# Performance work log

Measured on AMD Instinct MI355X. Metric: run time of the kernel, lower is better.

The kernel has to match this reference:

```python
import jax, jax.numpy as jnp
import numpy as np

# ---- config (mirrors cfg / init kwargs) ----
FEAT_STRIDE = 16
IM_DIMS = (1024, 1024)          # (height, width)
ANCHOR_SCALES = (8, 16, 32)
ANCHOR_RATIOS = (0.5, 1.0, 2.0)
PRE_NMS_TOPN = 6000             # eval mode (cfg_key=1)
POST_NMS_TOPN = 300
NMS_THRESH = 0.7
MIN_SIZE = 16


def _generate_base_anchors(base_size=16, ratios=ANCHOR_RATIOS, scales=ANCHOR_SCALES):
    """py-faster-rcnn generate_anchors, in numpy (static)."""
    def mk(ws, hs, xc, yc):
        return np.stack([xc - 0.5 * (ws - 1), yc - 0.5 * (hs - 1),
                         xc + 0.5 * (ws - 1), yc + 0.5 * (hs - 1)], axis=1)
    base = np.array([0, 0, base_size - 1, base_size - 1], dtype=np.float64)
    w = base[2] - base[0] + 1; h = base[3] - base[1] + 1
    xc = base[0] + 0.5 * (w - 1); yc = base[1] + 0.5 * (h - 1)
    # ratio enum
    size = w * h
    ws = np.round(np.sqrt(size / np.array(ratios)))
    hs = np.round(ws * np.array(ratios))
    ratio_anchors = mk(ws, hs, xc, yc)
    # scale enum
    out = []
    for a in ratio_anchors:
        aw = a[2] - a[0] + 1; ah = a[3] - a[1] + 1
        axc = a[0] + 0.5 * (aw - 1); ayc = a[1] + 0.5 * (ah - 1)
        out.append(mk(aw * np.array(scales), ah * np.array(scales), axc, ayc))
    return np.concatenate(out, axis=0).astype(np.float32)  # [A,4]


def _all_anchors(H, W):
    base = _generate_base_anchors()                       # [A,4]
    sx = np.arange(W) * FEAT_STRIDE
    sy = np.arange(H) * FEAT_STRIDE
    sx, sy = np.meshgrid(sx, sy)
    shifts = np.stack([sx.ravel(), sy.ravel(), sx.ravel(), sy.ravel()], axis=1)  # [H*W,4]
    anchors = shifts[:, None, :].astype(np.float32) + base[None, :, :]
    return anchors.reshape(-1, 4)                         # [H*W*A, 4]


def setup_inputs() -> dict:
    key = jax.random.key(0)
    k1, k2 = jax.random.split(key)
    H, W, A = 64, 64, 9
    rpn_cls_score = jax.random.normal(k1, (1, H, W, 2 * A), dtype=jnp.float32)
    rpn_bbox_pred = jax.random.normal(k2, (1, H, W, 4 * A), dtype=jnp.float32)
    return {"rpn_cls_score": rpn_cls_score, "rpn_bbox_pred": rpn_bbox_pred}


def _proposals(rpn_cls_score, rpn_bbox_pred):
    _, H, W, C2 = rpn_cls_score.shape
    A = C2 // 2
    # rpn_softmax: per-anchor 2-way softmax, foreground prob
    scores = jax.nn.softmax(rpn_cls_score.reshape(H, W, A, 2), axis=-1)[..., 1].reshape(-1)  # [N]
    deltas = rpn_bbox_pred.reshape(-1, 4)                  # [N,4]
    anchors = jnp.asarray(_all_anchors(H, W))              # [N,4]
    # bbox_transform_inv
    aw = anchors[:, 2] - anchors[:, 0] + 1.0
    ah = anchors[:, 3] - anchors[:, 1] + 1.0
    axc = anchors[:, 0] + 0.5 * aw
    ayc = anchors[:, 1] + 0.5 * ah
    dx, dy, dw, dh = deltas[:, 0], deltas[:, 1], deltas[:, 2], deltas[:, 3]
    pxc = dx * aw + axc; pyc = dy * ah + ayc
    pw = jnp.exp(dw) * aw; ph = jnp.exp(dh) * ah
    x1 = pxc - 0.5 * pw; y1 = pyc - 0.5 * ph
    x2 = pxc + 0.5 * pw; y2 = pyc + 0.5 * ph
    # clip to image
    im_h, im_w = IM_DIMS
    x1 = jnp.clip(x1, 0.0, im_w - 1.0); x2 = jnp.clip(x2, 0.0, im_w - 1.0)
    y1 = jnp.clip(y1, 0.0, im_h - 1.0); y2 = jnp.clip(y2, 0.0, im_h - 1.0)
    boxes = jnp.stack([x1, y1, x2, y2], axis=1)            # [N,4]
    # filter too-small boxes by masking their score
    valid = ((x2 - x1 + 1.0) >= MIN_SIZE) & ((y2 - y1 + 1.0) >= MIN_SIZE)
    scores = jnp.where(valid, scores, -jnp.inf)
    return boxes, scores


def _nms_keep(boxes, K):
    """Greedy NMS keep-mask over score-descending boxes [K,4]."""
    x1, y1, x2, y2 = boxes[:, 0], boxes[:, 1], boxes[:, 2], boxes[:, 3]
    areas = (x2 - x1 + 1.0) * (y2 - y1 + 1.0)
    ix1 = jnp.maximum(x1[:, None], x1[None, :])
    iy1 = jnp.maximum(y1[:, None], y1[None, :])
    ix2 = jnp.minimum(x2[:, None], x2[None, :])
    iy2 = jnp.minimum(y2[:, None], y2[None, :])
    iw = jnp.maximum(ix2 - ix1 + 1.0, 0.0)
    ih = jnp.maximum(iy2 - iy1 + 1.0, 0.0)
    inter = iw * ih
    iou = inter / (areas[:, None] + areas[None, :] - inter)  # [K,K]
    idxs = jnp.arange(K)
    def body(i, keep):
        sup = keep[i] & (iou[i] > NMS_THRESH) & (idxs > i)
        return keep & ~sup
    return jax.lax.fori_loop(0, K, body, jnp.ones((K,), bool))


def reference(rpn_cls_score, rpn_bbox_pred):
    boxes, scores = _proposals(rpn_cls_score, rpn_bbox_pred)
    K = min(PRE_NMS_TOPN, scores.shape[0])
    top_scores, order = jax.lax.top_k(scores, K)           # score-descending
    top_boxes = boxes[order]                               # [K,4]
    keep = _nms_keep(top_boxes, K)
    sel_scores = jnp.where(keep, top_scores, -jnp.inf)
    _, idx = jax.lax.top_k(sel_scores, POST_NMS_TOPN)      # kept, in score order
    out_boxes = top_boxes[idx]                             # [post,4]
    blob = jnp.concatenate([jnp.zeros((POST_NMS_TOPN, 1), out_boxes.dtype), out_boxes], axis=1)
    return blob                                            # [post,5] (batch_idx, x1,y1,x2,y2)
```

## Files before the change

### kernel.cpp

```cpp
#include <hip/hip_runtime.h>
#include <stdint.h>

typedef unsigned long long u64;
typedef unsigned int u32;

#define N_ANCH 36864
#define WGRID 64
#define A_PER 9
#define KTOP 6000
#define NOUT 300
#define NBIN 5120
#define NCHK 94
#define NCH2 47
#define NJ   6016
#define INF_BIN 0
#define NMSW 4
#define SLOTS 10
#define SPILLCAP 64

#define BARRIER_LDS() do {                                   \
    asm volatile("s_waitcnt lgkmcnt(0)" ::: "memory");       \
    __builtin_amdgcn_s_barrier();                            \
    asm volatile("" ::: "memory");                           \
} while (0)

__constant__ float c_ax1[9] = {-84.f,-176.f,-360.f,-56.f,-120.f,-248.f,-36.f,-80.f,-168.f};
__constant__ float c_ay1[9] = {-40.f,-88.f,-184.f,-56.f,-120.f,-248.f,-80.f,-168.f,-344.f};
__constant__ float c_aw[9]  = {184.f,368.f,736.f,128.f,256.f,512.f,88.f,176.f,352.f};
__constant__ float c_ah[9]  = {96.f,192.f,384.f,128.f,256.f,512.f,176.f,352.f,704.f};

__device__ __forceinline__ u32 binof(u32 u) {
    if (u < 0x80000000u) return 0u;
    if (u < 0xBF000000u) return 1u + ((u - 0x80000000u) >> 22);
    return 256u + ((u - 0xBF000000u) >> 11);
}

__global__ __launch_bounds__(256) void proposal_kernel(const float* __restrict__ cls,
                                                       const float* __restrict__ dlt,
                                                       u64* __restrict__ keys,
                                                       float4* __restrict__ boxes,
                                                       u32* __restrict__ hist) {
    __shared__ u32 lh[NBIN];
    const int t = threadIdx.x;
    for (int b = t; b < NBIN; b += 256) lh[b] = 0;
    __syncthreads();

    int i = blockIdx.x * 256 + t;
    int a  = i % A_PER;
    int hw = i / A_PER;
    int wx = hw % WGRID;
    int hy = hw / WGRID;

    float2 lp = *(const float2*)(cls + hw * 18 + 2 * a);
    float l0 = lp.x, l1 = lp.y;
    float m  = fmaxf(l0, l1);
    float e0 = expf(l0 - m), e1 = expf(l1 - m);
    float s  = e1 / (e0 + e1);

    float4 dd = *(const float4*)(dlt + hw * 36 + 4 * a);
    float dx = dd.x, dy = dd.y, dw = dd.z, dh = dd.w;
    float aw = c_aw[a], ah = c_ah[a];
    float axc = (c_ax1[a] + 16.f * (float)wx) + 0.5f * aw;
    float ayc = (c_ay1[a] + 16.f * (float)hy) + 0.5f * ah;

    float pxc = dx * aw + axc;
    float pyc = dy * ah + ayc;
    float pw  = expf(dw) * aw;
    float ph  = expf(dh) * ah;
    float x1 = pxc - 0.5f * pw, y1 = pyc - 0.5f * ph;
    float x2 = pxc + 0.5f * pw, y2 = pyc + 0.5f * ph;
    x1 = fminf(fmaxf(x1, 0.f), 1023.f);
    x2 = fminf(fmaxf(x2, 0.f), 1023.f);
    y1 = fminf(fmaxf(y1, 0.f), 1023.f);
    y2 = fminf(fmaxf(y2, 0.f), 1023.f);
    bool valid = ((x2 - x1 + 1.f) >= 16.f) && ((y2 - y1 + 1.f) >= 16.f);
    float sc = valid ? s : -__builtin_huge_valf();

    u32 sb  = __float_as_uint(sc);
    u32 ord = (sb & 0x80000000u) ? ~sb : (sb | 0x80000000u);
    u64 key = ((u64)ord << 32) | (u32)(~(u32)i);
    keys[i]  = key;
    boxes[i] = make_float4(x1, y1, x2, y2);

    u64 infb = __ballot(!valid);
    if (valid) {
        atomicAdd(&lh[binof(ord)], 1u);
    } else {
        int lane = t & 63;
        if (lane == __builtin_ctzll(infb))
            atomicAdd(&lh[INF_BIN], (u32)__popcll(infb));
    }
    __syncthreads();
    for (int b = t; b < NBIN; b += 256) {
        u32 v = lh[b];
        if (v) atomicAdd(&hist[b], v);
    }
}

__global__ __launch_bounds__(1024) void scan_kernel(const u32* __restrict__ hist,
                                                    u32* __restrict__ binStart,
                                                    u32* __restrict__ gEV) {
    __shared__ u32 wsum[16];
    const int t = threadIdx.x;
    const int lane = t & 63;
    const int v = t >> 6;
    if (t == 0) gEV[1] = KTOP;
    int hi = NBIN - 1 - 5 * t;
    u32 cnt[5];
    u32 sum = 0;
#pragma unroll
    for (int k = 0; k < 5; ++k) { cnt[k] = hist[hi - k]; sum += cnt[k]; }
    u32 s = sum;
#pragma unroll
    for (int d = 1; d < 64; d <<= 1) {
        u32 x = __shfl_up(s, d, 64);
        if (lane >= d) s += x;
    }
    if (lane == 63) wsum[v] = s;
    __syncthreads();
    u32 base = 0;
#pragma unroll
    for (int q = 0; q < 16; ++q) {
        u32 x = wsum[q];
        if (q < v) base += x;
    }
    u32 run = base + s - sum;
#pragma unroll
    for (int k = 0; k < 5; ++k) {
        int b = hi - k;
        binStart[b] = run;
        u32 end = run + cnt[k];
        if (run < KTOP && end >= KTOP) gEV[0] = end;
        run = end;
    }
}

__global__ void scatter_kernel(const u64* __restrict__ keys,
                               const u32* __restrict__ binStart,
                               u32* __restrict__ cursor,
                               u64* __restrict__ scat) {
    int i = blockIdx.x * blockDim.x + threadIdx.x;
    if (i >= N_ANCH) return;
    u64 k = keys[i];
    u32 b = binof((u32)(k >> 32));
    u32 s = binStart[b];
    if (s < KTOP) {
        u32 p = s + atomicAdd(&cursor[b], 1u);
        scat[p] = k;
    }
}

__global__ void rank_kernel(const u64* __restrict__ scat,
                            const u32* __restrict__ binStart,
                            const u32* __restrict__ hist,
                            const float4* __restrict__ boxes,
                            const u32* __restrict__ gEV,
                            float4* __restrict__ topBoxes,
                            int* __restrict__ gV) {
    int i = blockIdx.x * blockDim.x + threadIdx.x;
    u32 E = gEV[0];
    if (i >= (int)E) return;
    u64 k = scat[i];
    u32 b = binof((u32)(k >> 32));
    u32 s = binStart[b], c = hist[b];
    u32 r = s;
    for (u32 j = s; j < s + c; ++j) r += (scat[j] > k) ? 1u : 0u;
    if (r < KTOP) {
        int idx = (int)(~(u32)k);
        topBoxes[r] = boxes[idx];
        if (!(k >> 63)) atomicMin(gV, (int)r);
    }
}

__device__ __forceinline__ bool iou_gt(float4 a, float areaA, float4 b, float areaB) {
    float ix1 = fmaxf(a.x, b.x), iy1 = fmaxf(a.y, b.y);
    float ix2 = fminf(a.z, b.z), iy2 = fminf(a.w, b.w);
    float iw = fmaxf(ix2 - ix1 + 1.0f, 0.0f);
    float ih = fmaxf(iy2 - iy1 + 1.0f, 0.0f);
    float inter = iw * ih;
    float iou = inter / (areaA + areaB - inter);
    return iou > 0.7f;
}

__global__ __launch_bounds__(256) void maskT_kernel(const float4* __restrict__ topBoxes,
                                                    const u32* __restrict__ gEV,
                                                    u64* __restrict__ S) {
    const int V = (int)gEV[1];
    const int nch = (V + 63) >> 6;
    const int jc = blockIdx.x;
    const int w0 = blockIdx.y * 4;
    if (jc >= nch || w0 > jc) return;
    __shared__ float4 cb[256];
    __shared__ float  ca[256];
    const int t = threadIdx.x;
    const int lane = t & 63;
    {
        int ci = w0 * 64 + t;
        float4 b = (ci < V) ? topBoxes[ci] : make_float4(0.f, 0.f, -8.f, -8.f);
        cb[t] = b;
        ca[t] = (b.z - b.x + 1.f) * (b.w - b.y + 1.f);
    }
    __syncthreads();
    const int w = w0 + (t >> 6);
    if (w > jc || w >= nch) return;
    const int j = jc * 64 + lane;
    float4 bj = (j < V) ? topBoxes[j] : make_float4(0.f, 0.f, -8.f, -8.f);
    float aj = (bj.z - bj.x + 1.f) * (bj.w - bj.y + 1.f);
    const int s0 = (t >> 6) * 64;
    u64 m = 0;
#pragma unroll 4
    for (int b = 0; b < 64; ++b)
        if (iou_gt(bj, aj, cb[s0 + b], ca[s0 + b])) m |= (1ull << b);
    if (w == jc) m &= ((1ull << lane) - 1ull);
    S[(u64)w * NJ + j] = m;
}

__global__ __launch_bounds__(256) void nms_out_kernel(const float4* __restrict__ topBoxes,
                                                      const u32* __restrict__ gEV,
                                                      const u64* __restrict__ S,
                                                      float* __restrict__ out) {
    __shared__ u64 dA[NCH2][64];
    __shared__ u64 dAB[NCH2][64];
    __shared__ u64 dB[NCH2][64];
    __shared__ u64 keepw[NCHK];
    __shared__ u64 supw[2][2 * NMSW];
    __shared__ u64 spillK[SPILLCAP];
    __shared__ u32 spillW[SPILLCAP];
    __shared__ u32 wsum[NMSW];
    const int t = threadIdx.x;
    const int lane = t & 63;
    const int v = t >> 6;
    const int V = (int)gEV[1];
    const int nch = (V + 63) >> 6;
    const int nr  = (nch + 1) >> 1;
    if (t < NCHK) keepw[t] = 0;
    for (int idx = t; idx < nr * 64; idx += 256) {
        int r = idx >> 6, l = idx & 63;
        dA[r][l]  = S[(u64)(2 * r) * NJ + 128 * r + l];
        dAB[r][l] = S[(u64)(2 * r) * NJ + 128 * r + 64 + l];
        dB[r][l]  = S[(u64)(2 * r + 1) * NJ + 128 * r + 64 + l];
    }
    __syncthreads();

    u64 kwS[SLOTS], pA[SLOTS], pB[SLOTS], aofs[SLOTS];
#pragma unroll
    for (int k = 0; k < SLOTS; ++k) { kwS[k] = 0; pA[k] = 0; pB[k] = 0; aofs[k] = 0; }
    int nslot = 0, nspill = 0, nkept = 0;

    for (int r = 0; r < nr; ++r) {
        const int par = r & 1;
        u64 accA = 0, accB = 0;
#pragma unroll
        for (int k = 0; k < SLOTS; ++k) {
            if (nslot > NMSW * k + v) { accA |= pA[k] & kwS[k]; accB |= pB[k] & kwS[k]; }
        }
        for (int s = v; s < nspill; s += NMSW) {
            u64 kk = spillK[s];
            const u64* row = S + (u64)spillW[s] * NJ + 128 * r + lane;
            accA |= row[0] & kk; accB |= row[64] & kk;
        }
        u64 bA = __ballot(accA != 0ull), bB = __ballot(accB != 0ull);
        if (lane == 0) { supw[par][v] = bA; supw[par][NMSW + v] = bB; }
        if (r + 1 < nr) {
            u64 ofsn = (u64)(128 * (r + 1)) + lane;
#pragma unroll
            for (int k = 0; k < SLOTS; ++k)
                if (nslot > NMSW * k + v) { pA[k] = S[aofs[k] + ofsn]; pB[k] = S[aofs[k] + ofsn + 64]; }
        }
        BARRIER_LDS();
        u64 rwA = supw[par][0] | supw[par][1] | supw[par][2] | supw[par][3];
        u64 rwB = supw[par][4] | supw[par][5] | supw[par][6] | supw[par][7];
        int remA = V - 128 * r;
        int remB = remA - 64;
        u64 aliveA = (remA >= 64) ? ~0ull : ((remA <= 0) ? 0ull : ((1ull << remA) - 1ull));
        u64 aliveB = (remB >= 64) ? ~0ull : ((remB <= 0) ? 0ull : ((1ull << remB) - 1ull));
        u64 dAl = dA[r][lane], dABl = dAB[r][lane], dBl = dB[r][lane];
        u64 candA = ~rwA & aliveA, kbA = 0;
        while (candA) {
            int b = __builtin_ctzll(candA);
            kbA |= (1ull << b);
            candA &= ~(1ull << b);
            candA &= ~__ballot(((dAl >> b) & 1ull) != 0ull);
        }
        u64 supAB = __ballot((dABl & kbA) != 0ull);
        u64 candB = ~(rwB | supAB) & aliveB, kbB = 0;
        while (candB) {
            int b = __builtin_ctzll(candB);
            kbB |= (1ull << b);
            candB &= ~(1ull << b);
            candB &= ~__ballot(((dBl >> b) & 1ull) != 0ull);
        }
        if (t == 0) { keepw[2 * r] = kbA; if (2 * r + 1 < nch) keepw[2 * r + 1] = kbB; }
        bool sadd = false;
        if (kbA) {
            int so = nslot & (NMSW - 1), si = nslot >> 2;
            if (si < SLOTS) {
                if (v == so) {
#pragma unroll
                    for (int k = 0; k < SLOTS; ++k) if (k == si) {
                        kwS[k] = kbA; aofs[k] = (u64)(2 * r) * NJ;
                        if (r + 1 < nr) {
                            u64 o = (u64)(128 * (r + 1)) + lane;
                            pA[k] = S[aofs[k] + o]; pB[k] = S[aofs[k] + o + 64];
                        }
                    }
                }
                ++nslot;
            } else if (nspill < SPILLCAP) {
                if (v == NMSW - 1 && lane == 0) { spillW[nspill] = 2 * r; spillK[nspill] = kbA; }
                ++nspill; sadd = true;
            }
        }
        if (kbB) {
            int so = nslot & (NMSW - 1), si = nslot >> 2;
            if (si < SLOTS) {
                if (v == so) {
#pragma unroll
                    for (int k = 0; k < SLOTS; ++k) if (k == si) {
                        kwS[k] = kbB; aofs[k] = (u64)(2 * r + 1) * NJ;
                        if (r + 1 < nr) {
                            u64 o = (u64)(128 * (r + 1)) + lane;
                            pA[k] = S[aofs[k] + o]; pB[k] = S[aofs[k] + o + 64];
                        }
                    }
                }
                ++nslot;
            } else if (nspill < SPILLCAP) {
                if (v == NMSW - 1 && lane == 0) { spillW[nspill] = 2 * r + 1; spillK[nspill] = kbB; }
                ++nspill; sadd = true;
            }
        }
        if (sadd) BARRIER_LDS();
        nkept += __popcll(kbA) + __popcll(kbB);
        if (nkept >= NOUT) break;
    }
    __syncthreads();

    const int per = 24;
    int r0 = t * per;
    int r1 = min(r0 + per, KTOP);
    u32 cnt = 0;
    for (int r = r0; r < r1; ++r)
        cnt += (u32)((keepw[r >> 6] >> (r & 63)) & 1ull);
    u32 s = cnt;
#pragma unroll
    for (int d = 1; d < 64; d <<= 1) {
        u32 x = __shfl_up(s, d, 64);
        if (lane >= d) s += x;
    }
    if (lane == 63) wsum[v] = s;
    __syncthreads();
    u32 base = 0;
    u32 total = 0;
#pragma unroll
    for (int q = 0; q < NMSW; ++q) {
        u32 x = wsum[q];
        if (q < v) base += x;
        total += x;
    }
    const int n1 = min((int)total, NOUT);
    int kp = (int)(base + s - cnt);
    for (int r = r0; r < r1; ++r) {
        int kept = (int)((keepw[r >> 6] >> (r & 63)) & 1ull);
        int pos = kept ? kp : (n1 + r - kp);
        if (pos < NOUT) {
            float4 b = topBoxes[r];
            out[pos * 5 + 0] = 0.f;
            out[pos * 5 + 1] = b.x;
            out[pos * 5 + 2] = b.y;
            out[pos * 5 + 3] = b.z;
            out[pos * 5 + 4] = b.w;
        }
        kp += kept;
    }
}

extern "C" void kernel_launch(void* const* d_in, const int* in_sizes, int n_in,
                              void* d_out, int out_size, void* d_ws, size_t ws_size,
                              hipStream_t stream) {
    const float* cls = (const float*)d_in[0];
    const float* dlt = (const float*)d_in[1];
    float* out = (float*)d_out;
    char* ws = (char*)d_ws;
    u64*    keys     = (u64*)   (ws);
    u64*    scat     = (u64*)   (ws + 294912);
    float4* boxes    = (float4*)(ws + 589824);
    float4* topBoxes = (float4*)(ws + 1179648);
    u32*    hist     = (u32*)   (ws + 1275648);
    u32*    cursor   = (u32*)   (ws + 1296128);
    u32*    binStart = (u32*)   (ws + 1316608);
    u32*    gEV      = (u32*)   (ws + 1337088);
    u64*    S        = (u64*)   (ws + 1337344);

    hipMemsetAsync(hist, 0, 2 * NBIN * sizeof(u32), stream);
    proposal_kernel<<<144, 256, 0, stream>>>(cls, dlt, keys, boxes, hist);
    scan_kernel<<<1, 1024, 0, stream>>>(hist, binStart, gEV);
    scatter_kernel<<<(N_ANCH + 255) / 256, 256, 0, stream>>>(keys, binStart, cursor, scat);
    rank_kernel<<<(N_ANCH + 255) / 256, 256, 0, stream>>>(scat, binStart, hist, boxes, gEV,
                                                          topBoxes, (int*)&gEV[1]);
    maskT_kernel<<<dim3(NCHK, (NCHK + 3) / 4), 256, 0, stream>>>(topBoxes, gEV, S);
    nms_out_kernel<<<1, 256, 0, stream>>>(topBoxes, gEV, S, out);
}
```

Measured before the change: 120.7 us.

## Fuse all proposal/NMS stages into one cooperative kernel with grid syncs

Replaces the memset plus six separate kernel launches with a single cooperative kernel of 144 blocks that runs every stage (proposal, histogram scan, scatter, rank, mask build, NMS/output) separated by grid-wide syncs. The goal is to remove per-launch overhead and inter-kernel gaps, which dominate such a small, latency-bound pipeline. The mask stage now uses a triangular task list with wave shuffles instead of LDS staging. The NMS loop holds slots in named registers and prefetches the diagonal blocks instead of preloading them into LDS. If the cooperative launch fails, it falls back to per-phase launches. Grid syncs have their own cost, and fewer blocks are now used for the mask stage.

```diff
diff --git a/kernel.cpp b/kernel.cpp
--- a/kernel.cpp
+++ b/kernel.cpp
@@ -1,5 +1,8 @@
 #include <hip/hip_runtime.h>
+#include <hip/hip_cooperative_groups.h>
 #include <stdint.h>
+
+namespace cg = cooperative_groups;
 
 typedef unsigned long long u64;
 typedef unsigned int u32;
@@ -11,11 +14,9 @@
 #define NOUT 300
 #define NBIN 5120
 #define NCHK 94
-#define NCH2 47
 #define NJ   6016
-#define INF_BIN 0
-#define NMSW 4
-#define SLOTS 10
+#define GRIDB 144
+#define NSLOT 12
 #define SPILLCAP 64
 
 #define BARRIER_LDS() do {                                   \
@@ -33,143 +34,6 @@
     if (u < 0x80000000u) return 0u;
     if (u < 0xBF000000u) return 1u + ((u - 0x80000000u) >> 22);
     return 256u + ((u - 0xBF000000u) >> 11);
-}
-
-__global__ __launch_bounds__(256) void proposal_kernel(const float* __restrict__ cls,
-                                                       const float* __restrict__ dlt,
-                                                       u64* __restrict__ keys,
-                                                       float4* __restrict__ boxes,
-                                                       u32* __restrict__ hist) {
-    __shared__ u32 lh[NBIN];
-    const int t = threadIdx.x;
-    for (int b = t; b < NBIN; b += 256) lh[b] = 0;
-    __syncthreads();
-
-    int i = blockIdx.x * 256 + t;
-    int a  = i % A_PER;
-    int hw = i / A_PER;
-    int wx = hw % WGRID;
-    int hy = hw / WGRID;
-
-    float2 lp = *(const float2*)(cls + hw * 18 + 2 * a);
-    float l0 = lp.x, l1 = lp.y;
-    float m  = fmaxf(l0, l1);
-    float e0 = expf(l0 - m), e1 = expf(l1 - m);
-    float s  = e1 / (e0 + e1);
-
-    float4 dd = *(const float4*)(dlt + hw * 36 + 4 * a);
-    float dx = dd.x, dy = dd.y, dw = dd.z, dh = dd.w;
-    float aw = c_aw[a], ah = c_ah[a];
-    float axc = (c_ax1[a] + 16.f * (float)wx) + 0.5f * aw;
-    float ayc = (c_ay1[a] + 16.f * (float)hy) + 0.5f * ah;
-
-    float pxc = dx * aw + axc;
-    float pyc = dy * ah + ayc;
-    float pw  = expf(dw) * aw;
-    float ph  = expf(dh) * ah;
-    float x1 = pxc - 0.5f * pw, y1 = pyc - 0.5f * ph;
-    float x2 = pxc + 0.5f * pw, y2 = pyc + 0.5f * ph;
-    x1 = fminf(fmaxf(x1, 0.f), 1023.f);
-    x2 = fminf(fmaxf(x2, 0.f), 1023.f);
-    y1 = fminf(fmaxf(y1, 0.f), 1023.f);
-    y2 = fminf(fmaxf(y2, 0.f), 1023.f);
-    bool valid = ((x2 - x1 + 1.f) >= 16.f) && ((y2 - y1 + 1.f) >= 16.f);
-    float sc = valid ? s : -__builtin_huge_valf();
-
-    u32 sb  = __float_as_uint(sc);
-    u32 ord = (sb & 0x80000000u) ? ~sb : (sb | 0x80000000u);
-    u64 key = ((u64)ord << 32) | (u32)(~(u32)i);
-    keys[i]  = key;
-    boxes[i] = make_float4(x1, y1, x2, y2);
-
-    u64 infb = __ballot(!valid);
-    if (valid) {
-        atomicAdd(&lh[binof(ord)], 1u);
-    } else {
-        int lane = t & 63;
-        if (lane == __builtin_ctzll(infb))
-            atomicAdd(&lh[INF_BIN], (u32)__popcll(infb));
-    }
-    __syncthreads();
-    for (int b = t; b < NBIN; b += 256) {
-        u32 v = lh[b];
-        if (v) atomicAdd(&hist[b], v);
-    }
-}
-
-__global__ __launch_bounds__(1024) void scan_kernel(const u32* __restrict__ hist,
-                                                    u32* __restrict__ binStart,
-                                                    u32* __restrict__ gEV) {
-    __shared__ u32 wsum[16];
-    const int t = threadIdx.x;
-    const int lane = t & 63;
-    const int v = t >> 6;
-    if (t == 0) gEV[1] = KTOP;
-    int hi = NBIN - 1 - 5 * t;
-    u32 cnt[5];
-    u32 sum = 0;
-#pragma unroll
-    for (int k = 0; k < 5; ++k) { cnt[k] = hist[hi - k]; sum += cnt[k]; }
-    u32 s = sum;
-#pragma unroll
-    for (int d = 1; d < 64; d <<= 1) {
-        u32 x = __shfl_up(s, d, 64);
-        if (lane >= d) s += x;
-    }
-    if (lane == 63) wsum[v] = s;
-    __syncthreads();
-    u32 base = 0;
-#pragma unroll
-    for (int q = 0; q < 16; ++q) {
-        u32 x = wsum[q];
-        if (q < v) base += x;
-    }
-    u32 run = base + s - sum;
-#pragma unroll
-    for (int k = 0; k < 5; ++k) {
-        int b = hi - k;
-        binStart[b] = run;
-        u32 end = run + cnt[k];
-        if (run < KTOP && end >= KTOP) gEV[0] = end;
-        run = end;
-    }
-}
-
-__global__ void scatter_kernel(const u64* __restrict__ keys,
-                               const u32* __restrict__ binStart,
-                               u32* __restrict__ cursor,
-                               u64* __restrict__ scat) {
-    int i = blockIdx.x * blockDim.x + threadIdx.x;
-    if (i >= N_ANCH) return;
-    u64 k = keys[i];
-    u32 b = binof((u32)(k >> 32));
-    u32 s = binStart[b];
-    if (s < KTOP) {
-        u32 p = s + atomicAdd(&cursor[b], 1u);
-        scat[p] = k;
-    }
-}
-
-__global__ void rank_kernel(const u64* __restrict__ scat,
-                            const u32* __restrict__ binStart,
-                            const u32* __restrict__ hist,
-                            const float4* __restrict__ boxes,
-                            const u32* __restrict__ gEV,
-                            float4* __restrict__ topBoxes,
-                            int* __restrict__ gV) {
-    int i = blockIdx.x * blockDim.x + threadIdx.x;
-    u32 E = gEV[0];
-    if (i >= (int)E) return;
-    u64 k = scat[i];
-    u32 b = binof((u32)(k >> 32));
-    u32 s = binStart[b], c = hist[b];
-    u32 r = s;
-    for (u32 j = s; j < s + c; ++j) r += (scat[j] > k) ? 1u : 0u;
-    if (r < KTOP) {
-        int idx = (int)(~(u32)k);
-        topBoxes[r] = boxes[idx];
-        if (!(k >> 63)) atomicMin(gV, (int)r);
-    }
 }
 
 __device__ __forceinline__ bool iou_gt(float4 a, float areaA, float4 b, float areaB) {
@@ -182,206 +46,36 @@
     return iou > 0.7f;
 }
 
-__global__ __launch_bounds__(256) void maskT_kernel(const float4* __restrict__ topBoxes,
-                                                    const u32* __restrict__ gEV,
-                                                    u64* __restrict__ S) {
-    const int V = (int)gEV[1];
-    const int nch = (V + 63) >> 6;
-    const int jc = blockIdx.x;
-    const int w0 = blockIdx.y * 4;
-    if (jc >= nch || w0 > jc) return;
-    __shared__ float4 cb[256];
-    __shared__ float  ca[256];
-    const int t = threadIdx.x;
-    const int lane = t & 63;
-    {
-        int ci = w0 * 64 + t;
-        float4 b = (ci < V) ? topBoxes[ci] : make_float4(0.f, 0.f, -8.f, -8.f);
-        cb[t] = b;
-        ca[t] = (b.z - b.x + 1.f) * (b.w - b.y + 1.f);
-    }
-    __syncthreads();
-    const int w = w0 + (t >> 6);
-    if (w > jc || w >= nch) return;
-    const int j = jc * 64 + lane;
-    float4 bj = (j < V) ? topBoxes[j] : make_float4(0.f, 0.f, -8.f, -8.f);
-    float aj = (bj.z - bj.x + 1.f) * (bj.w - bj.y + 1.f);
-    const int s0 = (t >> 6) * 64;
-    u64 m = 0;
-#pragma unroll 4
-    for (int b = 0; b < 64; ++b)
-        if (iou_gt(bj, aj, cb[s0 + b], ca[s0 + b])) m |= (1ull << b);
-    if (w == jc) m &= ((1ull << lane) - 1ull);
-    S[(u64)w * NJ + j] = m;
-}
-
-__global__ __launch_bounds__(256) void nms_out_kernel(const float4* __restrict__ topBoxes,
-                                                      const u32* __restrict__ gEV,
-                                                      const u64* __restrict__ S,
-                                                      float* __restrict__ out) {
-    __shared__ u64 dA[NCH2][64];
-    __shared__ u64 dAB[NCH2][64];
-    __shared__ u64 dB[NCH2][64];
-    __shared__ u64 keepw[NCHK];
-    __shared__ u64 supw[2][2 * NMSW];
-    __shared__ u64 spillK[SPILLCAP];
-    __shared__ u32 spillW[SPILLCAP];
-    __shared__ u32 wsum[NMSW];
-    const int t = threadIdx.x;
-    const int lane = t & 63;
-    const int v = t >> 6;
-    const int V = (int)gEV[1];
-    const int nch = (V + 63) >> 6;
-    const int nr  = (nch + 1) >> 1;
-    if (t < NCHK) keepw[t] = 0;
-    for (int idx = t; idx < nr * 64; idx += 256) {
-        int r = idx >> 6, l = idx & 63;
-        dA[r][l]  = S[(u64)(2 * r) * NJ + 128 * r + l];
-        dAB[r][l] = S[(u64)(2 * r) * NJ + 128 * r + 64 + l];
-        dB[r][l]  = S[(u64)(2 * r + 1) * NJ + 128 * r + 64 + l];
-    }
-    __syncthreads();
-
-    u64 kwS[SLOTS], pA[SLOTS], pB[SLOTS], aofs[SLOTS];
-#pragma unroll
-    for (int k = 0; k < SLOTS; ++k) { kwS[k] = 0; pA[k] = 0; pB[k] = 0; aofs[k] = 0; }
-    int nslot = 0, nspill = 0, nkept = 0;
-
-    for (int r = 0; r < nr; ++r) {
-        const int par = r & 1;
-        u64 accA = 0, accB = 0;
-#pragma unroll
-        for (int k = 0; k < SLOTS; ++k) {
-            if (nslot > NMSW * k + v) { accA |= pA[k] & kwS[k]; accB |= pB[k] & kwS[k]; }
-        }
-        for (int s = v; s < nspill; s += NMSW) {
-            u64 kk = spillK[s];
-            const u64* row = S + (u64)spillW[s] * NJ + 128 * r + lane;
-            accA |= row[0] & kk; accB |= row[64] & kk;
-        }
-        u64 bA = __ballot(accA != 0ull), bB = __ballot(accB != 0ull);
-        if (lane == 0) { supw[par][v] = bA; supw[par][NMSW + v] = bB; }
-        if (r + 1 < nr) {
-            u64 ofsn = (u64)(128 * (r + 1)) + lane;
-#pragma unroll
-            for (int k = 0; k < SLOTS; ++k)
-                if (nslot > NMSW * k + v) { pA[k] = S[aofs[k] + ofsn]; pB[k] = S[aofs[k] + ofsn + 64]; }
-        }
-        BARRIER_LDS();
-        u64 rwA = supw[par][0] | supw[par][1] | supw[par][2] | supw[par][3];
-        u64 rwB = supw[par][4] | supw[par][5] | supw[par][6] | supw[par][7];
-        int remA = V - 128 * r;
-        int remB = remA - 64;
-        u64 aliveA = (remA >= 64) ? ~0ull : ((remA <= 0) ? 0ull : ((1ull << remA) - 1ull));
-        u64 aliveB = (remB >= 64) ? ~0ull : ((remB <= 0) ? 0ull : ((1ull << remB) - 1ull));
-        u64 dAl = dA[r][lane], dABl = dAB[r][lane], dBl = dB[r][lane];
-        u64 candA = ~rwA & aliveA, kbA = 0;
-        while (candA) {
-            int b = __builtin_ctzll(candA);
-            kbA |= (1ull << b);
-            candA &= ~(1ull << b);
-            candA &= ~__ballot(((dAl >> b) & 1ull) != 0ull);
-        }
-        u64 supAB = __ballot((dABl & kbA) != 0ull);
-        u64 candB = ~(rwB | supAB) & aliveB, kbB = 0;
-        while (candB) {
-            int b = __builtin_ctzll(candB);
-            kbB |= (1ull << b);
-            candB &= ~(1ull << b);
-            candB &= ~__ballot(((dBl >> b) & 1ull) != 0ull);
-        }
-        if (t == 0) { keepw[2 * r] = kbA; if (2 * r + 1 < nch) keepw[2 * r + 1] = kbB; }
-        bool sadd = false;
-        if (kbA) {
-            int so = nslot & (NMSW - 1), si = nslot >> 2;
-            if (si < SLOTS) {
-                if (v == so) {
-#pragma unroll
-                    for (int k = 0; k < SLOTS; ++k) if (k == si) {
-                        kwS[k] = kbA; aofs[k] = (u64)(2 * r) * NJ;
-                        if (r + 1 < nr) {
-                            u64 o = (u64)(128 * (r + 1)) + lane;
-                            pA[k] = S[aofs[k] + o]; pB[k] = S[aofs[k] + o + 64];
-                        }
-                    }
-                }
-                ++nslot;
-            } else if (nspill < SPILLCAP) {
-                if (v == NMSW - 1 && lane == 0) { spillW[nspill] = 2 * r; spillK[nspill] = kbA; }
-                ++nspill; sadd = true;
-            }
-        }
-        if (kbB) {
-            int so = nslot & (NMSW - 1), si = nslot >> 2;
-            if (si < SLOTS) {
-                if (v == so) {
-#pragma unroll
-                    for (int k = 0; k < SLOTS; ++k) if (k == si) {
-                        kwS[k] = kbB; aofs[k] = (u64)(2 * r + 1) * NJ;
-                        if (r + 1 < nr) {
-                            u64 o = (u64)(128 * (r + 1)) + lane;
-                            pA[k] = S[aofs[k] + o]; pB[k] = S[aofs[k] + o + 64];
-                        }
-                    }
-                }
-                ++nslot;
-            } else if (nspill < SPILLCAP) {
-                if (v == NMSW - 1 && lane == 0) { spillW[nspill] = 2 * r + 1; spillK[nspill] = kbB; }
-                ++nspill; sadd = true;
-            }
-        }
-        if (sadd) BARRIER_LDS();
-        nkept += __popcll(kbA) + __popcll(kbB);
-        if (nkept >= NOUT) break;
-    }
-    __syncthreads();
-
-    const int per = 24;
-    int r0 = t * per;
-    int r1 = min(r0 + per, KTOP);
-    u32 cnt = 0;
-    for (int r = r0; r < r1; ++r)
-        cnt += (u32)((keepw[r >> 6] >> (r & 63)) & 1ull);
-    u32 s = cnt;
-#pragma unroll
-    for (int d = 1; d < 64; d <<= 1) {
-        u32 x = __shfl_up(s, d, 64);
-        if (lane >= d) s += x;
-    }
-    if (lane == 63) wsum[v] = s;
-    __syncthreads();
-    u32 base = 0;
-    u32 total = 0;
-#pragma unroll
-    for (int q = 0; q < NMSW; ++q) {
-        u32 x = wsum[q];
-        if (q < v) base += x;
-        total += x;
-    }
-    const int n1 = min((int)total, NOUT);
-    int kp = (int)(base + s - cnt);
-    for (int r = r0; r < r1; ++r) {
-        int kept = (int)((keepw[r >> 6] >> (r & 63)) & 1ull);
-        int pos = kept ? kp : (n1 + r - kp);
-        if (pos < NOUT) {
-            float4 b = topBoxes[r];
-            out[pos * 5 + 0] = 0.f;
-            out[pos * 5 + 1] = b.x;
-            out[pos * 5 + 2] = b.y;
-            out[pos * 5 + 3] = b.z;
-            out[pos * 5 + 4] = b.w;
-        }
-        kp += kept;
-    }
-}
-
-extern "C" void kernel_launch(void* const* d_in, const int* in_sizes, int n_in,
-                              void* d_out, int out_size, void* d_ws, size_t ws_size,
-                              hipStream_t stream) {
-    const float* cls = (const float*)d_in[0];
-    const float* dlt = (const float*)d_in[1];
-    float* out = (float*)d_out;
-    char* ws = (char*)d_ws;
+#define SLOT_DECL(K) u64 kw##K = 0, pa##K = 0, pb##K = 0; u32 ao##K = 0;
+#define SLOT_ACC(K)  if (nslot > 4*(K) + v) { accA |= pa##K & kw##K; accB |= pb##K & kw##K; }
+#define SLOT_REF(K)  if (nslot > 4*(K) + v) { const u64* rp_ = S + (u64)ao##K * NJ + ofsn; pa##K = rp_[0]; pb##K = rp_[64]; }
+#define SLOT_CASE(K) case K: kw##K = kb_; ao##K = wch_; if (pf_) { const u64* rp_ = S + (u64)wch_ * NJ + onx_; pa##K = rp_[0]; pb##K = rp_[64]; } break;
+#define DO_CLAIM(KB, WCH) do {                                                \
+    u64 kb_ = (KB); u32 wch_ = (WCH);                                         \
+    int si_ = nslot >> 2, so_ = nslot & 3;                                    \
+    if (si_ < NSLOT) {                                                        \
+      if (v == so_) {                                                         \
+        bool pf_ = (r + 1 < nr);                                              \
+        u64 onx_ = (u64)(128 * (r + 1)) + lane;                               \
+        switch (si_) {                                                        \
+          SLOT_CASE(0) SLOT_CASE(1) SLOT_CASE(2) SLOT_CASE(3)                 \
+          SLOT_CASE(4) SLOT_CASE(5) SLOT_CASE(6) SLOT_CASE(7)                 \
+          SLOT_CASE(8) SLOT_CASE(9) SLOT_CASE(10) SLOT_CASE(11)               \
+          default: break;                                                     \
+        }                                                                     \
+      }                                                                       \
+      ++nslot;                                                                \
+    } else if (nspill < SPILLCAP) {                                           \
+      if (v == 3 && lane == 0) { sh.n.spillW[nspill] = wch_; sh.n.spillK[nspill] = kb_; } \
+      ++nspill; sadd = true;                                                  \
+    }                                                                         \
+  } while (0)
+
+__global__ __launch_bounds__(256) void fused_kernel(const float* __restrict__ cls,
+                                                    const float* __restrict__ dlt,
+                                                    float* __restrict__ out,
+                                                    char* __restrict__ ws,
+                                                    int ph) {
     u64*    keys     = (u64*)   (ws);
     u64*    scat     = (u64*)   (ws + 294912);
     float4* boxes    = (float4*)(ws + 589824);
@@ -392,12 +86,298 @@
     u32*    gEV      = (u32*)   (ws + 1337088);
     u64*    S        = (u64*)   (ws + 1337344);
 
-    hipMemsetAsync(hist, 0, 2 * NBIN * sizeof(u32), stream);
-    proposal_kernel<<<144, 256, 0, stream>>>(cls, dlt, keys, boxes, hist);
-    scan_kernel<<<1, 1024, 0, stream>>>(hist, binStart, gEV);
-    scatter_kernel<<<(N_ANCH + 255) / 256, 256, 0, stream>>>(keys, binStart, cursor, scat);
-    rank_kernel<<<(N_ANCH + 255) / 256, 256, 0, stream>>>(scat, binStart, hist, boxes, gEV,
-                                                          topBoxes, (int*)&gEV[1]);
-    maskT_kernel<<<dim3(NCHK, (NCHK + 3) / 4), 256, 0, stream>>>(topBoxes, gEV, S);
-    nms_out_kernel<<<1, 256, 0, stream>>>(topBoxes, gEV, S, out);
+    const int t = threadIdx.x;
+    const int bid = blockIdx.x;
+    const int gtid = bid * 256 + t;
+    const int lane = t & 63;
+    const int v = t >> 6;
+
+    __shared__ union ShU {
+        u32 lh[NBIN];
+        struct {
+            u64 keepw[NCHK];
+            u64 supw[2][8];
+            u64 spillK[SPILLCAP];
+            u32 spillW[SPILLCAP];
+            u32 wsum[4];
+        } n;
+    } sh;
+
+    if (ph < 0 || ph == 0) {
+        if (gtid < 2 * NBIN) hist[gtid] = 0;
+    }
+    if (ph < 0) cg::this_grid().sync();
+
+    if (ph < 0 || ph == 1) {
+        for (int b = t; b < NBIN; b += 256) sh.lh[b] = 0;
+        __syncthreads();
+
+        int i = gtid;
+        int a  = i % A_PER;
+        int hw = i / A_PER;
+        int wx = hw % WGRID;
+        int hy = hw / WGRID;
+
+        float2 lp = *(const float2*)(cls + hw * 18 + 2 * a);
+        float l0 = lp.x, l1 = lp.y;
+        float m  = fmaxf(l0, l1);
+        float e0 = expf(l0 - m), e1 = expf(l1 - m);
+        float s  = e1 / (e0 + e1);
+
+        float4 dd = *(const float4*)(dlt + hw * 36 + 4 * a);
+        float dx = dd.x, dy = dd.y, dw = dd.z, dh = dd.w;
+        float aw = c_aw[a], ah = c_ah[a];
+        float axc = (c_ax1[a] + 16.f * (float)wx) + 0.5f * aw;
+        float ayc = (c_ay1[a] + 16.f * (float)hy) + 0.5f * ah;
+
+        float pxc = dx * aw + axc;
+        float pyc = dy * ah + ayc;
+        float pw  = expf(dw) * aw;
+        float phh = expf(dh) * ah;
+        float x1 = pxc - 0.5f * pw, y1 = pyc - 0.5f * phh;
+        float x2 = pxc + 0.5f * pw, y2 = pyc + 0.5f * phh;
+        x1 = fminf(fmaxf(x1, 0.f), 1023.f);
+        x2 = fminf(fmaxf(x2, 0.f), 1023.f);
+        y1 = fminf(fmaxf(y1, 0.f), 1023.f);
+        y2 = fminf(fmaxf(y2, 0.f), 1023.f);
+        bool valid = ((x2 - x1 + 1.f) >= 16.f) && ((y2 - y1 + 1.f) >= 16.f);
+        float sc = valid ? s : -__builtin_huge_valf();
+
+        u32 sb  = __float_as_uint(sc);
+        u32 ord = (sb & 0x80000000u) ? ~sb : (sb | 0x80000000u);
+        u64 key = ((u64)ord << 32) | (u32)(~(u32)i);
+        keys[i]  = key;
+        boxes[i] = make_float4(x1, y1, x2, y2);
+
+        u64 infb = __ballot(!valid);
+        if (valid) {
+            atomicAdd(&sh.lh[binof(ord)], 1u);
+        } else {
+            if (lane == __builtin_ctzll(infb))
+                atomicAdd(&sh.lh[0], (u32)__popcll(infb));
+        }
+        __syncthreads();
+        for (int b = t; b < NBIN; b += 256) {
+            u32 x = sh.lh[b];
+            if (x) atomicAdd(&hist[b], x);
+        }
+    }
+    if (ph < 0) cg::this_grid().sync();
+
+    if ((ph < 0 || ph == 2) && bid == 0) {
+        if (t == 0) gEV[1] = KTOP;
+        int hi = NBIN - 1 - (NBIN / 256) * t;
+        u32 cnt[NBIN / 256];
+        u32 sum = 0;
+#pragma unroll
+        for (int k = 0; k < NBIN / 256; ++k) { cnt[k] = hist[hi - k]; sum += cnt[k]; }
+        u32 s = sum;
+#pragma unroll
+        for (int d = 1; d < 64; d <<= 1) {
+            u32 x = __shfl_up(s, d, 64);
+            if (lane >= d) s += x;
+        }
+        if (lane == 63) sh.n.wsum[v] = s;
+        __syncthreads();
+        u32 base = 0;
+#pragma unroll
+        for (int q = 0; q < 4; ++q) { u32 x = sh.n.wsum[q]; if (q < v) base += x; }
+        u32 run = base + s - sum;
+#pragma unroll
+        for (int k = 0; k < NBIN / 256; ++k) {
+            int b = hi - k;
+            binStart[b] = run;
+            u32 end = run + cnt[k];
+            if (run < KTOP && end >= KTOP) gEV[0] = end;
+            run = end;
+        }
+    }
+    if (ph < 0) cg::this_grid().sync();
+
+    if (ph < 0 || ph == 3) {
+        u64 k = keys[gtid];
+        u32 b = binof((u32)(k >> 32));
+        u32 s0 = binStart[b];
+        if (s0 < KTOP) {
+            u32 p = s0 + atomicAdd(&cursor[b], 1u);
+            scat[p] = k;
+        }
+    }
+    if (ph < 0) cg::this_grid().sync();
+
+    if (ph < 0 || ph == 4) {
+        u32 E = gEV[0];
+        if (gtid < (int)E) {
+            u64 k = scat[gtid];
+            u32 b = binof((u32)(k >> 32));
+            u32 s0 = binStart[b], c = hist[b];
+            u32 r = s0;
+            for (u32 j = s0; j < s0 + c; ++j) r += (scat[j] > k) ? 1u : 0u;
+            if (r < KTOP) {
+                int idx = (int)(~(u32)k);
+                topBoxes[r] = boxes[idx];
+                if (!(k >> 63)) atomicMin((int*)&gEV[1], (int)r);
+            }
+        }
+    }
+    if (ph < 0) cg::this_grid().sync();
+
+    if (ph < 0 || ph == 5) {
+        const int V = (int)gEV[1];
+        const int nch = (V + 63) >> 6;
+        const int ntask = nch * (nch + 1) / 2;
+        for (int tk = bid * 4 + v; tk < ntask; tk += GRIDB * 4) {
+            int jc = (int)((sqrtf(8.f * (float)tk + 1.f) - 1.f) * 0.5f);
+            while ((jc + 1) * (jc + 2) / 2 <= tk) ++jc;
+            while (jc * (jc + 1) / 2 > tk) --jc;
+            int w = tk - jc * (jc + 1) / 2;
+            int ci = w * 64 + lane;
+            float4 bi = (ci < V) ? topBoxes[ci] : make_float4(0.f, 0.f, -8.f, -8.f);
+            float ai = (bi.z - bi.x + 1.f) * (bi.w - bi.y + 1.f);
+            int j = jc * 64 + lane;
+            float4 bj = (j < V) ? topBoxes[j] : make_float4(0.f, 0.f, -8.f, -8.f);
+            float aj = (bj.z - bj.x + 1.f) * (bj.w - bj.y + 1.f);
+            u64 m = 0;
+#pragma unroll 4
+            for (int b = 0; b < 64; ++b) {
+                float4 bb;
+                bb.x = __shfl(bi.x, b, 64); bb.y = __shfl(bi.y, b, 64);
+                bb.z = __shfl(bi.z, b, 64); bb.w = __shfl(bi.w, b, 64);
+                float ab = __shfl(ai, b, 64);
+                if (iou_gt(bb, ab, bj, aj)) m |= (1ull << b);
+            }
+            if (w == jc) m &= ((1ull << lane) - 1ull);
+            S[(u64)w * NJ + j] = m;
+        }
+    }
+    if (ph < 0) cg::this_grid().sync();
+
+    if (!(ph < 0 || ph == 6)) return;
+    if (bid != 0) return;
+    {
+        const int V = (int)gEV[1];
+        const int nch = (V + 63) >> 6;
+        const int nr  = (nch + 1) >> 1;
+        if (t < NCHK) sh.n.keepw[t] = 0;
+
+        SLOT_DECL(0) SLOT_DECL(1) SLOT_DECL(2) SLOT_DECL(3)
+        SLOT_DECL(4) SLOT_DECL(5) SLOT_DECL(6) SLOT_DECL(7)
+        SLOT_DECL(8) SLOT_DECL(9) SLOT_DECL(10) SLOT_DECL(11)
+
+        u64 dAc  = S[lane];
+        u64 dABc = S[64 + lane];
+        u64 dBc  = S[(u64)NJ + 64 + lane];
+        int nslot = 0, nspill = 0, nkept = 0;
+
+        for (int r = 0; r < nr; ++r) {
+            const int par = r & 1;
+            u64 accA = 0, accB = 0;
+            SLOT_ACC(0) SLOT_ACC(1) SLOT_ACC(2) SLOT_ACC(3)
+            SLOT_ACC(4) SLOT_ACC(5) SLOT_ACC(6) SLOT_ACC(7)
+            SLOT_ACC(8) SLOT_ACC(9) SLOT_ACC(10) SLOT_ACC(11)
+            for (int s2 = v; s2 < nspill; s2 += 4) {
+                u64 kk = sh.n.spillK[s2];
+                const u64* row = S + (u64)sh.n.spillW[s2] * NJ + 128 * r + lane;
+                accA |= row[0] & kk; accB |= row[64] & kk;
+            }
+            u64 bA = __ballot(accA != 0ull), bB = __ballot(accB != 0ull);
+            if (lane == 0) { sh.n.supw[par][v] = bA; sh.n.supw[par][4 + v] = bB; }
+            u64 dAn = 0, dABn = 0, dBn = 0;
+            if (r + 1 < nr) {
+                u64 ofsn = (u64)(128 * (r + 1)) + lane;
+                SLOT_REF(0) SLOT_REF(1) SLOT_REF(2) SLOT_REF(3)
+                SLOT_REF(4) SLOT_REF(5) SLOT_REF(6) SLOT_REF(7)
+                SLOT_REF(8) SLOT_REF(9) SLOT_REF(10) SLOT_REF(11)
+                int rn = r + 1;
+                dAn  = S[(u64)(2 * rn) * NJ + 128 * rn + lane];
+                dABn = S[(u64)(2 * rn) * NJ + 128 * rn + 64 + lane];
+                dBn  = S[(u64)(2 * rn + 1) * NJ + 128 * rn + 64 + lane];
+            }
+            BARRIER_LDS();
+            u64 rwA = sh.n.supw[par][0] | sh.n.supw[par][1] | sh.n.supw[par][2] | sh.n.supw[par][3];
+            u64 rwB = sh.n.supw[par][4] | sh.n.supw[par][5] | sh.n.supw[par][6] | sh.n.supw[par][7];
+            int remA = V - 128 * r;
+            int remB = remA - 64;
+            u64 aliveA = (remA >= 64) ? ~0ull : ((remA <= 0) ? 0ull : ((1ull << remA) - 1ull));
+            u64 aliveB = (remB >= 64) ? ~0ull : ((remB <= 0) ? 0ull : ((1ull << remB) - 1ull));
+            u64 candA = ~rwA & aliveA, kbA = 0;
+            while (candA) {
+                int b = __builtin_ctzll(candA);
+                kbA |= (1ull << b);
+                candA &= ~(1ull << b);
+                candA &= ~__ballot(((dAc >> b) & 1ull) != 0ull);
+            }
+            u64 supAB = __ballot((dABc & kbA) != 0ull);
+            u64 candB = ~(rwB | supAB) & aliveB, kbB = 0;
+            while (candB) {
+                int b = __builtin_ctzll(candB);
+                kbB |= (1ull << b);
+                candB &= ~(1ull << b);
+                candB &= ~__ballot(((dBc >> b) & 1ull) != 0ull);
+            }
+            if (t == 0) { sh.n.keepw[2 * r] = kbA; if (2 * r + 1 < nch) sh.n.keepw[2 * r + 1] = kbB; }
+            bool sadd = false;
+            if (kbA) DO_CLAIM(kbA, (u32)(2 * r));
+            if (kbB) DO_CLAIM(kbB, (u32)(2 * r + 1));
+            if (sadd) BARRIER_LDS();
+            nkept += __popcll(kbA) + __popcll(kbB);
+            dAc = dAn; dABc = dABn; dBc = dBn;
+            if (nkept >= NOUT) break;
+        }
+        __syncthreads();
+
+        const int per = 24;
+        int r0 = t * per;
+        int r1 = min(r0 + per, KTOP);
+        u32 cnt2 = 0;
+        for (int rr = r0; rr < r1; ++rr)
+            cnt2 += (u32)((sh.n.keepw[rr >> 6] >> (rr & 63)) & 1ull);
+        u32 s2 = cnt2;
+#pragma unroll
+        for (int d = 1; d < 64; d <<= 1) {
+            u32 x = __shfl_up(s2, d, 64);
+            if (lane >= d) s2 += x;
+        }
+        if (lane == 63) sh.n.wsum[v] = s2;
+        __syncthreads();
+        u32 base = 0, total = 0;
+#pragma unroll
+        for (int q = 0; q < 4; ++q) {
+            u32 x = sh.n.wsum[q];
+            if (q < v) base += x;
+            total += x;
+        }
+        const int n1 = min((int)total, NOUT);
+        int kp = (int)(base + s2 - cnt2);
+        for (int rr = r0; rr < r1; ++rr) {
+            int kept = (int)((sh.n.keepw[rr >> 6] >> (rr & 63)) & 1ull);
+            int pos = kept ? kp : (n1 + rr - kp);
+            if (pos < NOUT) {
+                float4 b = topBoxes[rr];
+                out[pos * 5 + 0] = 0.f;
+                out[pos * 5 + 1] = b.x; out[pos * 5 + 2] = b.y;
+                out[pos * 5 + 3] = b.z; out[pos * 5 + 4] = b.w;
+            }
+            kp += kept;
+        }
+    }
 }
+
+extern "C" void kernel_launch(void* const* d_in, const int* in_sizes, int n_in,
+                              void* d_out, int out_size, void* d_ws, size_t ws_size,
+                              hipStream_t stream) {
+    const float* cls = (const float*)d_in[0];
+    const float* dlt = (const float*)d_in[1];
+    float* out = (float*)d_out;
+    char* ws = (char*)d_ws;
+
+    int ph = -1;
+    void* kargs[] = { (void*)&cls, (void*)&dlt, (void*)&out, (void*)&ws, (void*)&ph };
+    hipError_t e = hipLaunchCooperativeKernel((const void*)fused_kernel,
+                                              dim3(GRIDB), dim3(256), kargs, 0, stream);
+    if (e != hipSuccess) {
+        for (int p = 0; p <= 6; ++p)
+            hipLaunchKernelGGL(fused_kernel, dim3(GRIDB), dim3(256), 0, stream,
+                               cls, dlt, out, ws, p);
+    }
+}
```

Result: slower. 251.4 us (+108.3%).
